# Kernel optimization log

Measured on AMD Instinct MI355X. Metric: run time of the kernel, lower is better.

Reference implementation:

```python
import jax, jax.numpy as jnp
import numpy as np

HID = 128  # args['hidden_size']


def preprocess_adj(A):
    # A: [B, N, N] -> D^{-1/2} (A + I) D^{-1/2}
    N = A.shape[1]
    A_hat = A + jnp.eye(N, dtype=A.dtype)
    d = jnp.sum(A_hat, axis=2)                     # [B, N]
    d_safe = jnp.where(d > 0, d, 1.0)
    d_inv = jnp.where(d > 0, d_safe ** -0.5, 0.0)  # inf -> 0, as in torch code
    return d_inv[:, :, None] * A_hat * d_inv[:, None, :]


def lstm(x, w_ih, w_hh, b_ih, b_hh):
    # x: [B, T, H]; PyTorch gate order i, f, g, o; zero init state
    B = x.shape[0]
    H = w_hh.shape[1]
    def step(carry, xt):
        h, c = carry
        z = xt @ w_ih.T + b_ih + h @ w_hh.T + b_hh
        i, f, g, o = jnp.split(z, 4, axis=-1)
        c = jax.nn.sigmoid(f) * c + jax.nn.sigmoid(i) * jnp.tanh(g)
        h = jax.nn.sigmoid(o) * jnp.tanh(c)
        return (h, c), h
    h0 = jnp.zeros((B, H), x.dtype)
    c0 = jnp.zeros((B, H), x.dtype)
    _, hs = jax.lax.scan(step, (h0, c0), jnp.swapaxes(x, 0, 1))
    return jnp.swapaxes(hs, 0, 1)  # [B, T, H]


def gcn_dynamic_forward(x, A_norm, conv_w, conv_b, w_ih, w_hh, b_ih, b_hh):
    # x: [B, N, HID] with N >= HID: take last HID rows as dynamic-filter input
    df_in = x[:, x.shape[1] - HID:, :]              # [B, HID, HID]
    dyn = jax.lax.conv_general_dilated(
        df_in, conv_w, window_strides=(1,), padding=[(1, 1)],
        dimension_numbers=('NCH', 'OIH', 'NCH')) + conv_b[None, :, None]
    lw = lstm(dyn, w_ih, w_hh, b_ih, b_hh)          # [B, HID, HID]
    agg = jnp.matmul(A_norm, x)                     # [B, N, HID]
    out = jax.nn.sigmoid(jnp.matmul(agg, lw))       # output activation (1-layer GCN)
    return out                                       # dropout is identity in eval


def setup_inputs() -> dict:
    key = jax.random.key(0)
    ks = jax.random.split(key, 8)
    B, N = 4, 4096
    node_embedding = jax.random.normal(ks[0], (B, N, HID), dtype=jnp.float32)
    # sparse symmetric-ish 0/1 adjacency, avg degree ~ N*0.01
    adjacency_matrix = (jax.random.uniform(ks[1], (B, N, N)) < 0.01).astype(jnp.float32)
    s = 0.05
    conv_w = jax.random.normal(ks[2], (HID, HID, 3), dtype=jnp.float32) * s
    conv_b = jax.random.normal(ks[3], (HID,), dtype=jnp.float32) * s
    w_ih = jax.random.normal(ks[4], (4 * HID, HID), dtype=jnp.float32) * s
    w_hh = jax.random.normal(ks[5], (4 * HID, HID), dtype=jnp.float32) * s
    b_ih = jax.random.normal(ks[6], (4 * HID,), dtype=jnp.float32) * s
    b_hh = jax.random.normal(ks[7], (4 * HID,), dtype=jnp.float32) * s
    return {"node_embedding": node_embedding, "adjacency_matrix": adjacency_matrix,
            "conv_w": conv_w, "conv_b": conv_b,
            "w_ih": w_ih, "w_hh": w_hh, "b_ih": b_ih, "b_hh": b_hh}


def reference(node_embedding, adjacency_matrix, conv_w, conv_b, w_ih, w_hh, b_ih, b_hh):
    A_norm = preprocess_adj(adjacency_matrix)
    return gcn_dynamic_forward(node_embedding, A_norm, conv_w, conv_b, w_ih, w_hh, b_ih, b_hh)
```

## Files before the change

kernel.cpp:

```cpp
#include <hip/hip_runtime.h>
#include <math.h>

#define N_NODES 4096
#define HIDN 128
#define MAXNZ 128

typedef float v4f __attribute__((ext_vector_type(4)));
typedef _Float16 h2 __attribute__((ext_vector_type(2)));
typedef _Float16 h8 __attribute__((ext_vector_type(8)));

__device__ __forceinline__ float fsig(float x) { return 1.0f / (1.0f + __expf(-x)); }
__device__ __forceinline__ float ftanh_(float x) { return 1.0f - 2.0f / (__expf(2.0f * x) + 1.0f); }

__global__ __launch_bounds__(512) void k1_conv_ascan(
        const float* __restrict__ x, const float* __restrict__ conv_w,
        const float* __restrict__ conv_b, const float* __restrict__ w_ih,
        const float* __restrict__ b_ih, const float* __restrict__ b_hh,
        float* __restrict__ z3,
        const float* __restrict__ A, float* __restrict__ d_inv,
        int* __restrict__ cnt, int* __restrict__ idx) {
    __shared__ __align__(16) float dyn_lds[4][HIDN];
    __shared__ int sidx[8][MAXNZ];
    if (blockIdx.x < 128) {
        const int cb = blockIdx.x;
        const int b = cb >> 5;
        const int t0 = (cb & 31) * 4;
        const int tsub = threadIdx.x >> 7;
        const int h = threadIdx.x & 127;
        const int t = t0 + tsub;
        {
            const float* xb = x + ((size_t)b * N_NODES + (N_NODES - HIDN)) * HIDN;
            const float* w = conv_w + (size_t)t * HIDN * 3;
            float a0 = conv_b[t], a1 = 0.0f, a2 = 0.0f, a3 = 0.0f;
            #pragma unroll 4
            for (int i = 0; i < HIDN; i += 4) {
                const float* xr0 = xb + (size_t)i * HIDN;
                #pragma unroll
                for (int s = 0; s < 4; ++s) {
                    const float* xr = xr0 + s * HIDN;
                    float w0 = w[(i + s) * 3 + 0], w1 = w[(i + s) * 3 + 1], w2 = w[(i + s) * 3 + 2];
                    float left  = (h > 0)   ? xr[h - 1] : 0.0f;
                    float mid   = xr[h];
                    float right = (h < 127) ? xr[h + 1] : 0.0f;
                    if (s == 0)      a0 += left * w0 + mid * w1 + right * w2;
                    else if (s == 1) a1 += left * w0 + mid * w1 + right * w2;
                    else if (s == 2) a2 += left * w0 + mid * w1 + right * w2;
                    else             a3 += left * w0 + mid * w1 + right * w2;
                }
            }
            dyn_lds[tsub][h] = (a0 + a1) + (a2 + a3);
        }
        __syncthreads();
        const int u = threadIdx.x;
        const int qg = u >> 7;
        const int m  = u & 127;
        const float4* wr = (const float4*)(w_ih + (size_t)u * HIDN);
        float bias = b_ih[u] + b_hh[u];
        float acc0 = bias, acc1 = bias, acc2 = bias, acc3 = bias;
        #pragma unroll
        for (int half = 0; half < 2; ++half) {
            float4 wv[16];
            #pragma unroll
            for (int j = 0; j < 16; ++j) wv[j] = wr[half * 16 + j];
            const float4* d0 = (const float4*)dyn_lds[0] + half * 16;
            const float4* d1 = (const float4*)dyn_lds[1] + half * 16;
            const float4* d2 = (const float4*)dyn_lds[2] + half * 16;
            const float4* d3 = (const float4*)dyn_lds[3] + half * 16;
            #pragma unroll
            for (int j = 0; j < 16; ++j) {
                float4 wj = wv[j];
                float4 v0 = d0[j], v1 = d1[j], v2 = d2[j], v3 = d3[j];
                acc0 += wj.x * v0.x + wj.y * v0.y + wj.z * v0.z + wj.w * v0.w;
                acc1 += wj.x * v1.x + wj.y * v1.y + wj.z * v1.z + wj.w * v1.w;
                acc2 += wj.x * v2.x + wj.y * v2.y + wj.z * v2.z + wj.w * v2.w;
                acc3 += wj.x * v3.x + wj.y * v3.y + wj.z * v3.z + wj.w * v3.w;
            }
        }
        float* zb = z3 + (size_t)b * HIDN * HIDN * 4;
        zb[((size_t)(t0 + 0) * 128 + m) * 4 + qg] = acc0;
        zb[((size_t)(t0 + 1) * 128 + m) * 4 + qg] = acc1;
        zb[((size_t)(t0 + 2) * 128 + m) * 4 + qg] = acc2;
        zb[((size_t)(t0 + 3) * 128 + m) * 4 + qg] = acc3;
    } else {
        const int wid = threadIdx.x >> 6;
        const int lane = threadIdx.x & 63;
        const int r = (blockIdx.x - 128) * 8 + wid;
        const v4f* row = (const v4f*)(A + (size_t)r * N_NODES);
        const unsigned long long below = (1ull << lane) - 1ull;
        int cbase = 0;
        v4f cur[4], nxt[4];
        #pragma unroll
        for (int j = 0; j < 4; ++j) cur[j] = row[j * 64 + lane];
#define PROC1(c, col)                                                         \
        {                                                                     \
            bool nz = ((c) != 0.0f);                                          \
            unsigned long long mm = __ballot(nz);                             \
            if (mm) {                                                         \
                if (nz) {                                                     \
                    int p_ = cbase + __popcll(mm & below);                    \
                    if (p_ < MAXNZ) sidx[wid][p_] = (col);                    \
                }                                                             \
                cbase += __popcll(mm);                                        \
            }                                                                 \
        }
        #pragma unroll
        for (int g = 0; g < 4; ++g) {
            if (g < 3) {
                #pragma unroll
                for (int j = 0; j < 4; ++j) nxt[j] = row[(g + 1) * 256 + j * 64 + lane];
            }
            #pragma unroll
            for (int j = 0; j < 4; ++j) {
                int col0 = ((g * 4 + j) * 64 + lane) * 4;
                PROC1(cur[j].x, col0 + 0);
                PROC1(cur[j].y, col0 + 1);
                PROC1(cur[j].z, col0 + 2);
                PROC1(cur[j].w, col0 + 3);
            }
            #pragma unroll
            for (int j = 0; j < 4; ++j) cur[j] = nxt[j];
        }
#undef PROC1
        int cnt_r = (cbase < MAXNZ) ? cbase : MAXNZ;
        for (int k = lane; k < cnt_r; k += 64)
            idx[r * MAXNZ + k] = sidx[wid][k];
        if (lane == 0) {
            cnt[r] = cnt_r;
            d_inv[r] = rsqrtf((float)(cbase + 1));
        }
    }
}

__global__ __launch_bounds__(512, 2) void k2_lstm_gather(
        const float* __restrict__ z3, const float* __restrict__ w_hh,
        float* __restrict__ lw,
        const float* __restrict__ x, const float* __restrict__ d_inv,
        const int* __restrict__ cnt, const int* __restrict__ idx,
        float* __restrict__ agg) {
    __shared__ __align__(16) float4 zl[16 * 128];
    __shared__ __align__(16) _Float16 hbuf[2][HIDN];
    if (blockIdx.x < 4) {
        const int b = blockIdx.x;
        const int t = threadIdx.x;
        const int m = t >> 2;
        const int q = t & 3;
        h2 w2[4][16];
        #pragma unroll
        for (int g = 0; g < 4; ++g) {
            const float4* wr = (const float4*)(w_hh + ((size_t)(g * HIDN + m)) * HIDN + q * 32);
            #pragma unroll
            for (int j4 = 0; j4 < 8; ++j4) {
                float4 wv = wr[j4];
                w2[g][2 * j4 + 0] = h2{(_Float16)wv.x, (_Float16)wv.y};
                w2[g][2 * j4 + 1] = h2{(_Float16)wv.z, (_Float16)wv.w};
            }
        }
        float c = 0.0f;
        if (t < 64) ((h2*)hbuf[0])[t] = h2{(_Float16)0.0f, (_Float16)0.0f};
        const float4* zsrc = (const float4*)z3 + (size_t)b * 16384;
        float* lwb = lw + (size_t)b * HIDN * HIDN + m;
        float hist[4];
        for (int ch = 0; ch < 8; ++ch) {
            const float4* src = zsrc + ch * 2048;
            #pragma unroll
            for (int k = 0; k < 4; ++k)
                zl[t + 512 * k] = src[t + 512 * k];
            __syncthreads();
            #pragma unroll
            for (int si = 0; si < 16; ++si) {
                const int s = ch * 16 + si;
                const h8* hp = ((const h8*)hbuf[s & 1]) + q * 4;
                h8 H0 = hp[0], H1 = hp[1], H2 = hp[2], H3 = hp[3];
                h2 hh[16];
                #pragma unroll
                for (int j = 0; j < 4; ++j) {
                    hh[j]      = ((const h2*)&H0)[j];
                    hh[4 + j]  = ((const h2*)&H1)[j];
                    hh[8 + j]  = ((const h2*)&H2)[j];
                    hh[12 + j] = ((const h2*)&H3)[j];
                }
                float4 zv = zl[si * 128 + m];
                float a0 = 0.f, a1 = 0.f, a2 = 0.f, a3 = 0.f;
                #pragma unroll
                for (int j = 0; j < 16; ++j) {
                    a0 = __builtin_amdgcn_fdot2(w2[0][j], hh[j], a0, false);
                    a1 = __builtin_amdgcn_fdot2(w2[1][j], hh[j], a1, false);
                    a2 = __builtin_amdgcn_fdot2(w2[2][j], hh[j], a2, false);
                    a3 = __builtin_amdgcn_fdot2(w2[3][j], hh[j], a3, false);
                }
                a0 += __shfl_xor(a0, 1); a0 += __shfl_xor(a0, 2);
                a1 += __shfl_xor(a1, 1); a1 += __shfl_xor(a1, 2);
                a2 += __shfl_xor(a2, 1); a2 += __shfl_xor(a2, 2);
                a3 += __shfl_xor(a3, 1); a3 += __shfl_xor(a3, 2);
                float zi = a0 + zv.x;
                float zf = a1 + zv.y;
                float zg = a2 + zv.z;
                float zo = a3 + zv.w;
                float ig = fsig(zi);
                float fg = fsig(zf);
                float gg = ftanh_(zg);
                float og = fsig(zo);
                c = fg * c + ig * gg;
                float hn = og * ftanh_(c);
                if (q == (si & 3)) hist[si >> 2] = hn;
                if (q == 0) hbuf[(s + 1) & 1][m] = (_Float16)hn;
                __syncthreads();
            }
            #pragma unroll
            for (int j = 0; j < 4; ++j)
                lwb[(size_t)(ch * 16 + q + 4 * j) * HIDN] = hist[j];
        }
    } else {
        const int gIdx = blockIdx.x - 4;
        const int b = (gIdx & 7) >> 1;
        const int o = ((gIdx >> 3) << 1) | (gIdx & 1);
        const int wid = threadIdx.x >> 6;
        const int lane = threadIdx.x & 63;
        float* dl = (float*)zl;
        {
            const float4* dsrc = (const float4*)(d_inv + (b << 12));
            float4* ddst = (float4*)dl;
            ddst[threadIdx.x] = dsrc[threadIdx.x];
            ddst[threadIdx.x + 512] = dsrc[threadIdx.x + 512];
        }
        __syncthreads();
        const int i = o * 8 + wid;
        const int r = (b << 12) + i;
        const float2* xb = (const float2*)(x + (size_t)b * N_NODES * HIDN);
        const int* irow = idx + r * MAXNZ;
        const int n = cnt[r];
        float ax = 0.0f, ay = 0.0f;
        int k = 0;
        for (; k + 8 <= n; k += 8) {
            int4 j0 = *(const int4*)&irow[k];
            int4 j1 = *(const int4*)&irow[k + 4];
            float2 v0 = xb[(size_t)j0.x * 64 + lane];
            float2 v1 = xb[(size_t)j0.y * 64 + lane];
            float2 v2 = xb[(size_t)j0.z * 64 + lane];
            float2 v3 = xb[(size_t)j0.w * 64 + lane];
            float2 v4 = xb[(size_t)j1.x * 64 + lane];
            float2 v5 = xb[(size_t)j1.y * 64 + lane];
            float2 v6 = xb[(size_t)j1.z * 64 + lane];
            float2 v7 = xb[(size_t)j1.w * 64 + lane];
            float d0 = dl[j0.x], d1 = dl[j0.y], d2 = dl[j0.z], d3 = dl[j0.w];
            float d4 = dl[j1.x], d5 = dl[j1.y], d6 = dl[j1.z], d7 = dl[j1.w];
            ax += d0 * v0.x + d1 * v1.x + d2 * v2.x + d3 * v3.x
                + d4 * v4.x + d5 * v5.x + d6 * v6.x + d7 * v7.x;
            ay += d0 * v0.y + d1 * v1.y + d2 * v2.y + d3 * v3.y
                + d4 * v4.y + d5 * v5.y + d6 * v6.y + d7 * v7.y;
        }
        for (; k < n; ++k) {
            int j = irow[k];
            float dj = dl[j];
            float2 v = xb[(size_t)j * 64 + lane];
            ax += dj * v.x;
            ay += dj * v.y;
        }
        float di = dl[i];
        float2 vi = xb[(size_t)i * 64 + lane];
        float2 o2;
        o2.x = di * (ax + di * vi.x);
        o2.y = di * (ay + di * vi.y);
        ((float2*)(agg + (size_t)r * HIDN))[lane] = o2;
    }
}

__global__ __launch_bounds__(256) void k_outmm(
        const float* __restrict__ agg, const float* __restrict__ lw,
        float* __restrict__ out) {
    __shared__ __align__(16) float lw_lds[HIDN * HIDN];
    const int i0 = blockIdx.x * 64;
    const int b = i0 >> 12;
    const float4* lwg = (const float4*)(lw + (size_t)b * HIDN * HIDN);
    float4* lds4 = (float4*)lw_lds;
    for (int v = threadIdx.x; v < HIDN * HIDN / 4; v += 256) lds4[v] = lwg[v];
    __syncthreads();
    const int r0 = i0 + (threadIdx.x >> 3) * 2;
    const int u0 = (threadIdx.x & 7) * 16;
    const float4* a4 = (const float4*)agg;
    float4 acc[2][4];
    #pragma unroll
    for (int rr = 0; rr < 2; ++rr)
        #pragma unroll
        for (int cc = 0; cc < 4; ++cc) acc[rr][cc] = make_float4(0.f, 0.f, 0.f, 0.f);
    for (int f4 = 0; f4 < 32; ++f4) {
        float4 a0 = a4[(size_t)r0 * 32 + f4];
        float4 a1 = a4[(size_t)(r0 + 1) * 32 + f4];
        #pragma unroll
        for (int ff = 0; ff < 4; ++ff) {
            float af0 = (ff == 0) ? a0.x : (ff == 1) ? a0.y : (ff == 2) ? a0.z : a0.w;
            float af1 = (ff == 0) ? a1.x : (ff == 1) ? a1.y : (ff == 2) ? a1.z : a1.w;
            int f = f4 * 4 + ff;
            const float4* wrow = (const float4*)(lw_lds + f * HIDN + u0);
            #pragma unroll
            for (int cc = 0; cc < 4; ++cc) {
                float4 wv = wrow[cc];
                acc[0][cc].x += af0 * wv.x; acc[0][cc].y += af0 * wv.y;
                acc[0][cc].z += af0 * wv.z; acc[0][cc].w += af0 * wv.w;
                acc[1][cc].x += af1 * wv.x; acc[1][cc].y += af1 * wv.y;
                acc[1][cc].z += af1 * wv.z; acc[1][cc].w += af1 * wv.w;
            }
        }
    }
    #pragma unroll
    for (int rr = 0; rr < 2; ++rr) {
        #pragma unroll
        for (int cc = 0; cc < 4; ++cc) {
            float4 ov;
            ov.x = fsig(acc[rr][cc].x);
            ov.y = fsig(acc[rr][cc].y);
            ov.z = fsig(acc[rr][cc].z);
            ov.w = fsig(acc[rr][cc].w);
            *(float4*)(out + (size_t)(r0 + rr) * HIDN + u0 + cc * 4) = ov;
        }
    }
}

extern "C" void kernel_launch(void* const* d_in, const int* in_sizes, int n_in,
                              void* d_out, int out_size, void* d_ws, size_t ws_size,
                              hipStream_t stream) {
    const float* x      = (const float*)d_in[0];
    const float* A      = (const float*)d_in[1];
    const float* conv_w = (const float*)d_in[2];
    const float* conv_b = (const float*)d_in[3];
    const float* w_ih   = (const float*)d_in[4];
    const float* w_hh   = (const float*)d_in[5];
    const float* b_ih   = (const float*)d_in[6];
    const float* b_hh   = (const float*)d_in[7];
    float* out = (float*)d_out;

    char* ws = (char*)d_ws;
    float* d_inv = (float*)ws;
    int*   cnt   = (int*)(ws + 65536);
    int*   idx   = (int*)(ws + 131072);
    float* z3    = (float*)(ws + 131072 + 8388608);
    float* lw    = (float*)(ws + 131072 + 8388608 + 1048576);
    float* agg   = (float*)(ws + 131072 + 8388608 + 1048576 + 262144);

    hipLaunchKernelGGL(k1_conv_ascan, dim3(2176), dim3(512), 0, stream,
                       x, conv_w, conv_b, w_ih, b_ih, b_hh, z3, A, d_inv, cnt, idx);
    hipLaunchKernelGGL(k2_lstm_gather, dim3(2052), dim3(512), 0, stream,
                       z3, w_hh, lw, x, d_inv, cnt, idx, agg);
    hipLaunchKernelGGL(k_outmm, dim3(256), dim3(256), 0, stream, agg, lw, out);
}
```

Baseline: 500.7 us.

## Fuse three kernels into one cooperative persistent kernel with grid syncs

Replaces the three launches with a single cooperative kernel of 512 blocks that runs conv+input-projection and the adjacency scan, then the LSTM and neighbour gather, then the output matmul, separated by grid-wide syncs. Rows are strided across persistent warps instead of one row per warp per block. The aim is to remove launch gaps and inter-kernel drain. In exchange, the gather now reads d_inv from global memory instead of LDS, the output matmul computes one row per thread instead of two, and the three-kernel path is kept as a fallback. The serial LSTM still limits the middle phase while the other blocks wait at the grid barrier.

Result: slower. 840.0 us (+67.8%).

```diff
diff --git a/kernel.cpp b/kernel.cpp
--- a/kernel.cpp
+++ b/kernel.cpp
@@ -1,9 +1,14 @@
 #include <hip/hip_runtime.h>
+#include <hip/hip_cooperative_groups.h>
 #include <math.h>
+
+namespace cg = cooperative_groups;
 
 #define N_NODES 4096
 #define HIDN 128
 #define MAXNZ 128
+#define CGRID 512
+#define NTHR 512
 
 typedef float v4f __attribute__((ext_vector_type(4)));
 typedef _Float16 h2 __attribute__((ext_vector_type(2)));
@@ -12,308 +17,357 @@
 __device__ __forceinline__ float fsig(float x) { return 1.0f / (1.0f + __expf(-x)); }
 __device__ __forceinline__ float ftanh_(float x) { return 1.0f - 2.0f / (__expf(2.0f * x) + 1.0f); }
 
-__global__ __launch_bounds__(512) void k1_conv_ascan(
+
+__device__ __forceinline__ void convz_body(
+        int cb, int tid, const float* __restrict__ x,
+        const float* __restrict__ conv_w, const float* __restrict__ conv_b,
+        const float* __restrict__ w_ih, const float* __restrict__ b_ih,
+        const float* __restrict__ b_hh, float* __restrict__ z3,
+        float* dl ) {
+    const int b = cb >> 5;
+    const int t0 = (cb & 31) * 4;
+    const int tsub = tid >> 7;
+    const int h = tid & 127;
+    const int t = t0 + tsub;
+    {
+        const float* xb = x + ((size_t)b * N_NODES + (N_NODES - HIDN)) * HIDN;
+        const float* w = conv_w + (size_t)t * HIDN * 3;
+        float a0 = conv_b[t], a1 = 0.0f, a2 = 0.0f, a3 = 0.0f;
+        #pragma unroll 4
+        for (int i = 0; i < HIDN; i += 4) {
+            const float* xr0 = xb + (size_t)i * HIDN;
+            #pragma unroll
+            for (int s = 0; s < 4; ++s) {
+                const float* xr = xr0 + s * HIDN;
+                float w0 = w[(i + s) * 3 + 0], w1 = w[(i + s) * 3 + 1], w2 = w[(i + s) * 3 + 2];
+                float left  = (h > 0)   ? xr[h - 1] : 0.0f;
+                float mid   = xr[h];
+                float right = (h < 127) ? xr[h + 1] : 0.0f;
+                if (s == 0)      a0 += left * w0 + mid * w1 + right * w2;
+                else if (s == 1) a1 += left * w0 + mid * w1 + right * w2;
+                else if (s == 2) a2 += left * w0 + mid * w1 + right * w2;
+                else             a3 += left * w0 + mid * w1 + right * w2;
+            }
+        }
+        dl[tsub * HIDN + h] = (a0 + a1) + (a2 + a3);
+    }
+    __syncthreads();
+    const int u = tid;
+    const int qg = u >> 7;
+    const int m  = u & 127;
+    const float4* wr = (const float4*)(w_ih + (size_t)u * HIDN);
+    float bias = b_ih[u] + b_hh[u];
+    float acc0 = bias, acc1 = bias, acc2 = bias, acc3 = bias;
+    #pragma unroll
+    for (int half = 0; half < 2; ++half) {
+        float4 wv[16];
+        #pragma unroll
+        for (int j = 0; j < 16; ++j) wv[j] = wr[half * 16 + j];
+        const float4* d0 = (const float4*)(dl + 0 * HIDN) + half * 16;
+        const float4* d1 = (const float4*)(dl + 1 * HIDN) + half * 16;
+        const float4* d2 = (const float4*)(dl + 2 * HIDN) + half * 16;
+        const float4* d3 = (const float4*)(dl + 3 * HIDN) + half * 16;
+        #pragma unroll
+        for (int j = 0; j < 16; ++j) {
+            float4 wj = wv[j];
+            float4 v0 = d0[j], v1 = d1[j], v2 = d2[j], v3 = d3[j];
+            acc0 += wj.x * v0.x + wj.y * v0.y + wj.z * v0.z + wj.w * v0.w;
+            acc1 += wj.x * v1.x + wj.y * v1.y + wj.z * v1.z + wj.w * v1.w;
+            acc2 += wj.x * v2.x + wj.y * v2.y + wj.z * v2.z + wj.w * v2.w;
+            acc3 += wj.x * v3.x + wj.y * v3.y + wj.z * v3.z + wj.w * v3.w;
+        }
+    }
+    float* zb = z3 + (size_t)b * HIDN * HIDN * 4;
+    zb[((size_t)(t0 + 0) * 128 + m) * 4 + qg] = acc0;
+    zb[((size_t)(t0 + 1) * 128 + m) * 4 + qg] = acc1;
+    zb[((size_t)(t0 + 2) * 128 + m) * 4 + qg] = acc2;
+    zb[((size_t)(t0 + 3) * 128 + m) * 4 + qg] = acc3;
+}
+
+__device__ __forceinline__ void ascan_row(
+        int r, int lane, const float* __restrict__ A, float* __restrict__ d_inv,
+        int* __restrict__ cnt, int* __restrict__ idx, int* sidx_w) {
+    const v4f* row = (const v4f*)(A + (size_t)r * N_NODES);
+    const unsigned long long below = (1ull << lane) - 1ull;
+    int cbase = 0;
+    v4f cur[4], nxt[4];
+    #pragma unroll
+    for (int j = 0; j < 4; ++j) cur[j] = row[j * 64 + lane];
+#define PROC1(c, col)                                                         \
+    {                                                                         \
+        bool nz = ((c) != 0.0f);                                              \
+        unsigned long long mm = __ballot(nz);                                 \
+        if (mm) {                                                             \
+            if (nz) {                                                         \
+                int p_ = cbase + __popcll(mm & below);                        \
+                if (p_ < MAXNZ) sidx_w[p_] = (col);                           \
+            }                                                                 \
+            cbase += __popcll(mm);                                            \
+        }                                                                     \
+    }
+    #pragma unroll
+    for (int g = 0; g < 4; ++g) {
+        if (g < 3) {
+            #pragma unroll
+            for (int j = 0; j < 4; ++j) nxt[j] = row[(g + 1) * 256 + j * 64 + lane];
+        }
+        #pragma unroll
+        for (int j = 0; j < 4; ++j) {
+            int col0 = ((g * 4 + j) * 64 + lane) * 4;
+            PROC1(cur[j].x, col0 + 0);
+            PROC1(cur[j].y, col0 + 1);
+            PROC1(cur[j].z, col0 + 2);
+            PROC1(cur[j].w, col0 + 3);
+        }
+        #pragma unroll
+        for (int j = 0; j < 4; ++j) cur[j] = nxt[j];
+    }
+#undef PROC1
+    int cnt_r = (cbase < MAXNZ) ? cbase : MAXNZ;
+    for (int k = lane; k < cnt_r; k += 64)
+        idx[r * MAXNZ + k] = sidx_w[k];
+    if (lane == 0) {
+        cnt[r] = cnt_r;
+        d_inv[r] = rsqrtf((float)(cbase + 1));
+    }
+}
+
+__device__ __forceinline__ void lstm_body(
+        int b, int t, const float* __restrict__ z3, const float* __restrict__ w_hh,
+        float* __restrict__ lw, float4* zl, _Float16* hb) {
+    const int m = t >> 2;
+    const int q = t & 3;
+    h2 w2[4][16];
+    #pragma unroll
+    for (int g = 0; g < 4; ++g) {
+        const float4* wr = (const float4*)(w_hh + ((size_t)(g * HIDN + m)) * HIDN + q * 32);
+        #pragma unroll
+        for (int j4 = 0; j4 < 8; ++j4) {
+            float4 wv = wr[j4];
+            w2[g][2 * j4 + 0] = h2{(_Float16)wv.x, (_Float16)wv.y};
+            w2[g][2 * j4 + 1] = h2{(_Float16)wv.z, (_Float16)wv.w};
+        }
+    }
+    float c = 0.0f;
+    if (t < 64) ((h2*)hb)[t] = h2{(_Float16)0.0f, (_Float16)0.0f};
+    const float4* zsrc = (const float4*)z3 + (size_t)b * 16384;
+    float* lwb = lw + (size_t)b * HIDN * HIDN + m;
+    float hist[4];
+    for (int ch = 0; ch < 8; ++ch) {
+        const float4* src = zsrc + ch * 2048;
+        #pragma unroll
+        for (int k = 0; k < 4; ++k)
+            zl[t + 512 * k] = src[t + 512 * k];
+        __syncthreads();
+        #pragma unroll
+        for (int si = 0; si < 16; ++si) {
+            const int s = ch * 16 + si;
+            const h8* hp = ((const h8*)(hb + (size_t)(s & 1) * HIDN)) + q * 4;
+            h8 H0 = hp[0], H1 = hp[1], H2 = hp[2], H3 = hp[3];
+            float4 zv = zl[si * 128 + m];
+            float a0 = 0.f, a1 = 0.f, a2 = 0.f, a3 = 0.f;
+            #pragma unroll
+            for (int j = 0; j < 16; ++j) {
+                h2 hj = (j < 4)  ? ((const h2*)&H0)[j]
+                      : (j < 8)  ? ((const h2*)&H1)[j - 4]
+                      : (j < 12) ? ((const h2*)&H2)[j - 8]
+                                 : ((const h2*)&H3)[j - 12];
+                a0 = __builtin_amdgcn_fdot2(w2[0][j], hj, a0, false);
+                a1 = __builtin_amdgcn_fdot2(w2[1][j], hj, a1, false);
+                a2 = __builtin_amdgcn_fdot2(w2[2][j], hj, a2, false);
+                a3 = __builtin_amdgcn_fdot2(w2[3][j], hj, a3, false);
+            }
+            a0 += __shfl_xor(a0, 1); a0 += __shfl_xor(a0, 2);
+            a1 += __shfl_xor(a1, 1); a1 += __shfl_xor(a1, 2);
+            a2 += __shfl_xor(a2, 1); a2 += __shfl_xor(a2, 2);
+            a3 += __shfl_xor(a3, 1); a3 += __shfl_xor(a3, 2);
+            float zi = a0 + zv.x;
+            float zf = a1 + zv.y;
+            float zg = a2 + zv.z;
+            float zo = a3 + zv.w;
+            float ig = fsig(zi);
+            float fg = fsig(zf);
+            float gg = ftanh_(zg);
+            float og = fsig(zo);
+            c = fg * c + ig * gg;
+            float hn = og * ftanh_(c);
+            if (q == (si & 3)) hist[si >> 2] = hn;
+            if (q == 0) hb[(size_t)((s + 1) & 1) * HIDN + m] = (_Float16)hn;
+            __syncthreads();
+        }
+        #pragma unroll
+        for (int j = 0; j < 4; ++j)
+            lwb[(size_t)(ch * 16 + q + 4 * j) * HIDN] = hist[j];
+    }
+}
+
+__device__ __forceinline__ void gather_row(
+        int r, int lane, const float* __restrict__ x,
+        const float* __restrict__ d_inv, const int* __restrict__ cnt,
+        const int* __restrict__ idx, float* __restrict__ agg) {
+    const int b = r >> 12;
+    const int i = r & 4095;
+    const float* dv = d_inv + (b << 12);
+    const float2* xb = (const float2*)(x + (size_t)b * N_NODES * HIDN);
+    const int* irow = idx + r * MAXNZ;
+    const int n = cnt[r];
+    float ax = 0.0f, ay = 0.0f;
+    int k = 0;
+    for (; k + 8 <= n; k += 8) {
+        int4 j0 = *(const int4*)&irow[k];
+        int4 j1 = *(const int4*)&irow[k + 4];
+        float2 v0 = xb[(size_t)j0.x * 64 + lane];
+        float2 v1 = xb[(size_t)j0.y * 64 + lane];
+        float2 v2 = xb[(size_t)j0.z * 64 + lane];
+        float2 v3 = xb[(size_t)j0.w * 64 + lane];
+        float2 v4 = xb[(size_t)j1.x * 64 + lane];
+        float2 v5 = xb[(size_t)j1.y * 64 + lane];
+        float2 v6 = xb[(size_t)j1.z * 64 + lane];
+        float2 v7 = xb[(size_t)j1.w * 64 + lane];
+        float d0 = dv[j0.x], d1 = dv[j0.y], d2 = dv[j0.z], d3 = dv[j0.w];
+        float d4 = dv[j1.x], d5 = dv[j1.y], d6 = dv[j1.z], d7 = dv[j1.w];
+        ax += d0 * v0.x + d1 * v1.x + d2 * v2.x + d3 * v3.x
+            + d4 * v4.x + d5 * v5.x + d6 * v6.x + d7 * v7.x;
+        ay += d0 * v0.y + d1 * v1.y + d2 * v2.y + d3 * v3.y
+            + d4 * v4.y + d5 * v5.y + d6 * v6.y + d7 * v7.y;
+    }
+    for (; k < n; ++k) {
+        int j = irow[k];
+        float dj = dv[j];
+        float2 v = xb[(size_t)j * 64 + lane];
+        ax += dj * v.x;
+        ay += dj * v.y;
+    }
+    float di = dv[i];
+    float2 vi = xb[(size_t)i * 64 + lane];
+    float2 o2;
+    o2.x = di * (ax + di * vi.x);
+    o2.y = di * (ay + di * vi.y);
+    ((float2*)(agg + (size_t)r * HIDN))[lane] = o2;
+}
+
+__device__ __forceinline__ void outmm_body(
+        int bb, int tid, const float* __restrict__ agg,
+        const float* __restrict__ lw, float* __restrict__ out, float* lw_lds) {
+    const int i0 = bb * 64;
+    const int b = i0 >> 12;
+    const float4* lwg = (const float4*)(lw + (size_t)b * HIDN * HIDN);
+    float4* lds4 = (float4*)lw_lds;
+    for (int v = tid; v < HIDN * HIDN / 4; v += NTHR) lds4[v] = lwg[v];
+    __syncthreads();
+    const int r0 = i0 + (tid >> 3);
+    const int u0 = (tid & 7) * 16;
+    const float4* a4 = (const float4*)agg;
+    float4 acc[4];
+    #pragma unroll
+    for (int cc = 0; cc < 4; ++cc) acc[cc] = make_float4(0.f, 0.f, 0.f, 0.f);
+    for (int f4 = 0; f4 < 32; ++f4) {
+        float4 a0 = a4[(size_t)r0 * 32 + f4];
+        #pragma unroll
+        for (int ff = 0; ff < 4; ++ff) {
+            float af0 = (ff == 0) ? a0.x : (ff == 1) ? a0.y : (ff == 2) ? a0.z : a0.w;
+            const float4* wrow = (const float4*)(lw_lds + (f4 * 4 + ff) * HIDN + u0);
+            #pragma unroll
+            for (int cc = 0; cc < 4; ++cc) {
+                float4 wv = wrow[cc];
+                acc[cc].x += af0 * wv.x; acc[cc].y += af0 * wv.y;
+                acc[cc].z += af0 * wv.z; acc[cc].w += af0 * wv.w;
+            }
+        }
+    }
+    #pragma unroll
+    for (int cc = 0; cc < 4; ++cc) {
+        float4 ov;
+        ov.x = fsig(acc[cc].x);
+        ov.y = fsig(acc[cc].y);
+        ov.z = fsig(acc[cc].z);
+        ov.w = fsig(acc[cc].w);
+        *(float4*)(out + (size_t)r0 * HIDN + u0 + cc * 4) = ov;
+    }
+}
+
+__global__ __launch_bounds__(NTHR, 4) void k_fused(
+        const float* __restrict__ x, const float* __restrict__ A,
+        const float* __restrict__ conv_w, const float* __restrict__ conv_b,
+        const float* __restrict__ w_ih, const float* __restrict__ w_hh,
+        const float* __restrict__ b_ih, const float* __restrict__ b_hh,
+        float* __restrict__ z3, float* __restrict__ d_inv,
+        int* __restrict__ cnt, int* __restrict__ idx,
+        float* __restrict__ lw, float* __restrict__ agg,
+        float* __restrict__ out) {
+    __shared__ __align__(16) char arena[65536];
+    cg::grid_group grid = cg::this_grid();
+    const int tid = threadIdx.x;
+    const int bid = blockIdx.x;
+    const int wid = tid >> 6;
+    const int lane = tid & 63;
+
+    if (bid < 128) {
+        convz_body(bid, tid, x, conv_w, conv_b, w_ih, b_ih, b_hh, z3, (float*)arena);
+    } else {
+        int* sidx_w = (int*)arena + wid * MAXNZ;
+        const int gw = (bid - 128) * 8 + wid;
+        for (int r = gw; r < 16384; r += 3072)
+            ascan_row(r, lane, A, d_inv, cnt, idx, sidx_w);
+    }
+    __threadfence();
+    grid.sync();
+
+    if (bid < 4) {
+        lstm_body(bid, tid, z3, w_hh, lw, (float4*)arena, (_Float16*)(arena + 32768));
+    } else {
+        const int gw = (bid - 4) * 8 + wid;
+        for (int r = gw; r < 16384; r += 4064)
+            gather_row(r, lane, x, d_inv, cnt, idx, agg);
+    }
+    __threadfence();
+    grid.sync();
+
+    if (bid < 256)
+        outmm_body(bid, tid, agg, lw, out, (float*)arena);
+}
+
+__global__ __launch_bounds__(512) void k1_fb(
         const float* __restrict__ x, const float* __restrict__ conv_w,
         const float* __restrict__ conv_b, const float* __restrict__ w_ih,
         const float* __restrict__ b_ih, const float* __restrict__ b_hh,
         float* __restrict__ z3,
         const float* __restrict__ A, float* __restrict__ d_inv,
         int* __restrict__ cnt, int* __restrict__ idx) {
-    __shared__ __align__(16) float dyn_lds[4][HIDN];
-    __shared__ int sidx[8][MAXNZ];
+    __shared__ __align__(16) char arena[4096];
     if (blockIdx.x < 128) {
-        const int cb = blockIdx.x;
-        const int b = cb >> 5;
-        const int t0 = (cb & 31) * 4;
-        const int tsub = threadIdx.x >> 7;
-        const int h = threadIdx.x & 127;
-        const int t = t0 + tsub;
-        {
-            const float* xb = x + ((size_t)b * N_NODES + (N_NODES - HIDN)) * HIDN;
-            const float* w = conv_w + (size_t)t * HIDN * 3;
-            float a0 = conv_b[t], a1 = 0.0f, a2 = 0.0f, a3 = 0.0f;
-            #pragma unroll 4
-            for (int i = 0; i < HIDN; i += 4) {
-                const float* xr0 = xb + (size_t)i * HIDN;
-                #pragma unroll
-                for (int s = 0; s < 4; ++s) {
-                    const float* xr = xr0 + s * HIDN;
-                    float w0 = w[(i + s) * 3 + 0], w1 = w[(i + s) * 3 + 1], w2 = w[(i + s) * 3 + 2];
-                    float left  = (h > 0)   ? xr[h - 1] : 0.0f;
-                    float mid   = xr[h];
-                    float right = (h < 127) ? xr[h + 1] : 0.0f;
-                    if (s == 0)      a0 += left * w0 + mid * w1 + right * w2;
-                    else if (s == 1) a1 += left * w0 + mid * w1 + right * w2;
-                    else if (s == 2) a2 += left * w0 + mid * w1 + right * w2;
-                    else             a3 += left * w0 + mid * w1 + right * w2;
-                }
-            }
-            dyn_lds[tsub][h] = (a0 + a1) + (a2 + a3);
-        }
-        __syncthreads();
-        const int u = threadIdx.x;
-        const int qg = u >> 7;
-        const int m  = u & 127;
-        const float4* wr = (const float4*)(w_ih + (size_t)u * HIDN);
-        float bias = b_ih[u] + b_hh[u];
-        float acc0 = bias, acc1 = bias, acc2 = bias, acc3 = bias;
-        #pragma unroll
-        for (int half = 0; half < 2; ++half) {
-            float4 wv[16];
-            #pragma unroll
-            for (int j = 0; j < 16; ++j) wv[j] = wr[half * 16 + j];
-            const float4* d0 = (const float4*)dyn_lds[0] + half * 16;
-            const float4* d1 = (const float4*)dyn_lds[1] + half * 16;
-            const float4* d2 = (const float4*)dyn_lds[2] + half * 16;
-            const float4* d3 = (const float4*)dyn_lds[3] + half * 16;
-            #pragma unroll
-            for (int j = 0; j < 16; ++j) {
-                float4 wj = wv[j];
-                float4 v0 = d0[j], v1 = d1[j], v2 = d2[j], v3 = d3[j];
-                acc0 += wj.x * v0.x + wj.y * v0.y + wj.z * v0.z + wj.w * v0.w;
-                acc1 += wj.x * v1.x + wj.y * v1.y + wj.z * v1.z + wj.w * v1.w;
-                acc2 += wj.x * v2.x + wj.y * v2.y + wj.z * v2.z + wj.w * v2.w;
-                acc3 += wj.x * v3.x + wj.y * v3.y + wj.z * v3.z + wj.w * v3.w;
-            }
-        }
-        float* zb = z3 + (size_t)b * HIDN * HIDN * 4;
-        zb[((size_t)(t0 + 0) * 128 + m) * 4 + qg] = acc0;
-        zb[((size_t)(t0 + 1) * 128 + m) * 4 + qg] = acc1;
-        zb[((size_t)(t0 + 2) * 128 + m) * 4 + qg] = acc2;
-        zb[((size_t)(t0 + 3) * 128 + m) * 4 + qg] = acc3;
+        convz_body(blockIdx.x, threadIdx.x, x, conv_w, conv_b, w_ih, b_ih, b_hh,
+                   z3, (float*)arena);
     } else {
         const int wid = threadIdx.x >> 6;
         const int lane = threadIdx.x & 63;
-        const int r = (blockIdx.x - 128) * 8 + wid;
-        const v4f* row = (const v4f*)(A + (size_t)r * N_NODES);
-        const unsigned long long below = (1ull << lane) - 1ull;
-        int cbase = 0;
-        v4f cur[4], nxt[4];
-        #pragma unroll
-        for (int j = 0; j < 4; ++j) cur[j] = row[j * 64 + lane];
-#define PROC1(c, col)                                                         \
-        {                                                                     \
-            bool nz = ((c) != 0.0f);                                          \
-            unsigned long long mm = __ballot(nz);                             \
-            if (mm) {                                                         \
-                if (nz) {                                                     \
-                    int p_ = cbase + __popcll(mm & below);                    \
-                    if (p_ < MAXNZ) sidx[wid][p_] = (col);                    \
-                }                                                             \
-                cbase += __popcll(mm);                                        \
-            }                                                                 \
-        }
-        #pragma unroll
-        for (int g = 0; g < 4; ++g) {
-            if (g < 3) {
-                #pragma unroll
-                for (int j = 0; j < 4; ++j) nxt[j] = row[(g + 1) * 256 + j * 64 + lane];
-            }
-            #pragma unroll
-            for (int j = 0; j < 4; ++j) {
-                int col0 = ((g * 4 + j) * 64 + lane) * 4;
-                PROC1(cur[j].x, col0 + 0);
-                PROC1(cur[j].y, col0 + 1);
-                PROC1(cur[j].z, col0 + 2);
-                PROC1(cur[j].w, col0 + 3);
-            }
-            #pragma unroll
-            for (int j = 0; j < 4; ++j) cur[j] = nxt[j];
-        }
-#undef PROC1
-        int cnt_r = (cbase < MAXNZ) ? cbase : MAXNZ;
-        for (int k = lane; k < cnt_r; k += 64)
-            idx[r * MAXNZ + k] = sidx[wid][k];
-        if (lane == 0) {
-            cnt[r] = cnt_r;
-            d_inv[r] = rsqrtf((float)(cbase + 1));
-        }
-    }
-}
-
-__global__ __launch_bounds__(512, 2) void k2_lstm_gather(
+        int* sidx_w = (int*)arena + wid * MAXNZ;
+        ascan_row((blockIdx.x - 128) * 8 + wid, lane, A, d_inv, cnt, idx, sidx_w);
+    }
+}
+
+__global__ __launch_bounds__(512) void k2_fb(
         const float* __restrict__ z3, const float* __restrict__ w_hh,
         float* __restrict__ lw,
         const float* __restrict__ x, const float* __restrict__ d_inv,
         const int* __restrict__ cnt, const int* __restrict__ idx,
         float* __restrict__ agg) {
-    __shared__ __align__(16) float4 zl[16 * 128];
-    __shared__ __align__(16) _Float16 hbuf[2][HIDN];
+    __shared__ __align__(16) char arena[33280];
     if (blockIdx.x < 4) {
-        const int b = blockIdx.x;
-        const int t = threadIdx.x;
-        const int m = t >> 2;
-        const int q = t & 3;
-        h2 w2[4][16];
-        #pragma unroll
-        for (int g = 0; g < 4; ++g) {
-            const float4* wr = (const float4*)(w_hh + ((size_t)(g * HIDN + m)) * HIDN + q * 32);
-            #pragma unroll
-            for (int j4 = 0; j4 < 8; ++j4) {
-                float4 wv = wr[j4];
-                w2[g][2 * j4 + 0] = h2{(_Float16)wv.x, (_Float16)wv.y};
-                w2[g][2 * j4 + 1] = h2{(_Float16)wv.z, (_Float16)wv.w};
-            }
-        }
-        float c = 0.0f;
-        if (t < 64) ((h2*)hbuf[0])[t] = h2{(_Float16)0.0f, (_Float16)0.0f};
-        const float4* zsrc = (const float4*)z3 + (size_t)b * 16384;
-        float* lwb = lw + (size_t)b * HIDN * HIDN + m;
-        float hist[4];
-        for (int ch = 0; ch < 8; ++ch) {
-            const float4* src = zsrc + ch * 2048;
-            #pragma unroll
-            for (int k = 0; k < 4; ++k)
-                zl[t + 512 * k] = src[t + 512 * k];
-            __syncthreads();
-            #pragma unroll
-            for (int si = 0; si < 16; ++si) {
-                const int s = ch * 16 + si;
-                const h8* hp = ((const h8*)hbuf[s & 1]) + q * 4;
-                h8 H0 = hp[0], H1 = hp[1], H2 = hp[2], H3 = hp[3];
-                h2 hh[16];
-                #pragma unroll
-                for (int j = 0; j < 4; ++j) {
-                    hh[j]      = ((const h2*)&H0)[j];
-                    hh[4 + j]  = ((const h2*)&H1)[j];
-                    hh[8 + j]  = ((const h2*)&H2)[j];
-                    hh[12 + j] = ((const h2*)&H3)[j];
-                }
-                float4 zv = zl[si * 128 + m];
-                float a0 = 0.f, a1 = 0.f, a2 = 0.f, a3 = 0.f;
-                #pragma unroll
-                for (int j = 0; j < 16; ++j) {
-                    a0 = __builtin_amdgcn_fdot2(w2[0][j], hh[j], a0, false);
-                    a1 = __builtin_amdgcn_fdot2(w2[1][j], hh[j], a1, false);
-                    a2 = __builtin_amdgcn_fdot2(w2[2][j], hh[j], a2, false);
-                    a3 = __builtin_amdgcn_fdot2(w2[3][j], hh[j], a3, false);
-                }
-                a0 += __shfl_xor(a0, 1); a0 += __shfl_xor(a0, 2);
-                a1 += __shfl_xor(a1, 1); a1 += __shfl_xor(a1, 2);
-                a2 += __shfl_xor(a2, 1); a2 += __shfl_xor(a2, 2);
-                a3 += __shfl_xor(a3, 1); a3 += __shfl_xor(a3, 2);
-                float zi = a0 + zv.x;
-                float zf = a1 + zv.y;
-                float zg = a2 + zv.z;
-                float zo = a3 + zv.w;
-                float ig = fsig(zi);
-                float fg = fsig(zf);
-                float gg = ftanh_(zg);
-                float og = fsig(zo);
-                c = fg * c + ig * gg;
-                float hn = og * ftanh_(c);
-                if (q == (si & 3)) hist[si >> 2] = hn;
-                if (q == 0) hbuf[(s + 1) & 1][m] = (_Float16)hn;
-                __syncthreads();
-            }
-            #pragma unroll
-            for (int j = 0; j < 4; ++j)
-                lwb[(size_t)(ch * 16 + q + 4 * j) * HIDN] = hist[j];
-        }
+        lstm_body(blockIdx.x, threadIdx.x, z3, w_hh, lw,
+                  (float4*)arena, (_Float16*)(arena + 32768));
     } else {
-        const int gIdx = blockIdx.x - 4;
-        const int b = (gIdx & 7) >> 1;
-        const int o = ((gIdx >> 3) << 1) | (gIdx & 1);
         const int wid = threadIdx.x >> 6;
         const int lane = threadIdx.x & 63;
-        float* dl = (float*)zl;
-        {
-            const float4* dsrc = (const float4*)(d_inv + (b << 12));
-            float4* ddst = (float4*)dl;
-            ddst[threadIdx.x] = dsrc[threadIdx.x];
-            ddst[threadIdx.x + 512] = dsrc[threadIdx.x + 512];
-        }
-        __syncthreads();
-        const int i = o * 8 + wid;
-        const int r = (b << 12) + i;
-        const float2* xb = (const float2*)(x + (size_t)b * N_NODES * HIDN);
-        const int* irow = idx + r * MAXNZ;
-        const int n = cnt[r];
-        float ax = 0.0f, ay = 0.0f;
-        int k = 0;
-        for (; k + 8 <= n; k += 8) {
-            int4 j0 = *(const int4*)&irow[k];
-            int4 j1 = *(const int4*)&irow[k + 4];
-            float2 v0 = xb[(size_t)j0.x * 64 + lane];
-            float2 v1 = xb[(size_t)j0.y * 64 + lane];
-            float2 v2 = xb[(size_t)j0.z * 64 + lane];
-            float2 v3 = xb[(size_t)j0.w * 64 + lane];
-            float2 v4 = xb[(size_t)j1.x * 64 + lane];
-            float2 v5 = xb[(size_t)j1.y * 64 + lane];
-            float2 v6 = xb[(size_t)j1.z * 64 + lane];
-            float2 v7 = xb[(size_t)j1.w * 64 + lane];
-            float d0 = dl[j0.x], d1 = dl[j0.y], d2 = dl[j0.z], d3 = dl[j0.w];
-            float d4 = dl[j1.x], d5 = dl[j1.y], d6 = dl[j1.z], d7 = dl[j1.w];
-            ax += d0 * v0.x + d1 * v1.x + d2 * v2.x + d3 * v3.x
-                + d4 * v4.x + d5 * v5.x + d6 * v6.x + d7 * v7.x;
-            ay += d0 * v0.y + d1 * v1.y + d2 * v2.y + d3 * v3.y
-                + d4 * v4.y + d5 * v5.y + d6 * v6.y + d7 * v7.y;
-        }
-        for (; k < n; ++k) {
-            int j = irow[k];
-            float dj = dl[j];
-            float2 v = xb[(size_t)j * 64 + lane];
-            ax += dj * v.x;
-            ay += dj * v.y;
-        }
-        float di = dl[i];
-        float2 vi = xb[(size_t)i * 64 + lane];
-        float2 o2;
-        o2.x = di * (ax + di * vi.x);
-        o2.y = di * (ay + di * vi.y);
-        ((float2*)(agg + (size_t)r * HIDN))[lane] = o2;
-    }
-}
-
-__global__ __launch_bounds__(256) void k_outmm(
+        gather_row((blockIdx.x - 4) * 8 + wid, lane, x, d_inv, cnt, idx, agg);
+    }
+}
+
+__global__ __launch_bounds__(512) void k3_fb(
         const float* __restrict__ agg, const float* __restrict__ lw,
         float* __restrict__ out) {
-    __shared__ __align__(16) float lw_lds[HIDN * HIDN];
-    const int i0 = blockIdx.x * 64;
-    const int b = i0 >> 12;
-    const float4* lwg = (const float4*)(lw + (size_t)b * HIDN * HIDN);
-    float4* lds4 = (float4*)lw_lds;
-    for (int v = threadIdx.x; v < HIDN * HIDN / 4; v += 256) lds4[v] = lwg[v];
-    __syncthreads();
-    const int r0 = i0 + (threadIdx.x >> 3) * 2;
-    const int u0 = (threadIdx.x & 7) * 16;
-    const float4* a4 = (const float4*)agg;
-    float4 acc[2][4];
-    #pragma unroll
-    for (int rr = 0; rr < 2; ++rr)
-        #pragma unroll
-        for (int cc = 0; cc < 4; ++cc) acc[rr][cc] = make_float4(0.f, 0.f, 0.f, 0.f);
-    for (int f4 = 0; f4 < 32; ++f4) {
-        float4 a0 = a4[(size_t)r0 * 32 + f4];
-        float4 a1 = a4[(size_t)(r0 + 1) * 32 + f4];
-        #pragma unroll
-        for (int ff = 0; ff < 4; ++ff) {
-            float af0 = (ff == 0) ? a0.x : (ff == 1) ? a0.y : (ff == 2) ? a0.z : a0.w;
-            float af1 = (ff == 0) ? a1.x : (ff == 1) ? a1.y : (ff == 2) ? a1.z : a1.w;
-            int f = f4 * 4 + ff;
-            const float4* wrow = (const float4*)(lw_lds + f * HIDN + u0);
-            #pragma unroll
-            for (int cc = 0; cc < 4; ++cc) {
-                float4 wv = wrow[cc];
-                acc[0][cc].x += af0 * wv.x; acc[0][cc].y += af0 * wv.y;
-                acc[0][cc].z += af0 * wv.z; acc[0][cc].w += af0 * wv.w;
-                acc[1][cc].x += af1 * wv.x; acc[1][cc].y += af1 * wv.y;
-                acc[1][cc].z += af1 * wv.z; acc[1][cc].w += af1 * wv.w;
-            }
-        }
-    }
-    #pragma unroll
-    for (int rr = 0; rr < 2; ++rr) {
-        #pragma unroll
-        for (int cc = 0; cc < 4; ++cc) {
-            float4 ov;
-            ov.x = fsig(acc[rr][cc].x);
-            ov.y = fsig(acc[rr][cc].y);
-            ov.z = fsig(acc[rr][cc].z);
-            ov.w = fsig(acc[rr][cc].w);
-            *(float4*)(out + (size_t)(r0 + rr) * HIDN + u0 + cc * 4) = ov;
-        }
-    }
+    __shared__ __align__(16) char arena[65536];
+    outmm_body(blockIdx.x, threadIdx.x, agg, lw, out, (float*)arena);
 }
 
 extern "C" void kernel_launch(void* const* d_in, const int* in_sizes, int n_in,
@@ -337,9 +391,19 @@
     float* lw    = (float*)(ws + 131072 + 8388608 + 1048576);
     float* agg   = (float*)(ws + 131072 + 8388608 + 1048576 + 262144);
 
-    hipLaunchKernelGGL(k1_conv_ascan, dim3(2176), dim3(512), 0, stream,
-                       x, conv_w, conv_b, w_ih, b_ih, b_hh, z3, A, d_inv, cnt, idx);
-    hipLaunchKernelGGL(k2_lstm_gather, dim3(2052), dim3(512), 0, stream,
-                       z3, w_hh, lw, x, d_inv, cnt, idx, agg);
-    hipLaunchKernelGGL(k_outmm, dim3(256), dim3(256), 0, stream, agg, lw, out);
-}
+    void* args[] = {
+        (void*)&x, (void*)&A, (void*)&conv_w, (void*)&conv_b,
+        (void*)&w_ih, (void*)&w_hh, (void*)&b_ih, (void*)&b_hh,
+        (void*)&z3, (void*)&d_inv, (void*)&cnt, (void*)&idx,
+        (void*)&lw, (void*)&agg, (void*)&out,
+    };
+    hipError_t err = hipLaunchCooperativeKernel(
+        (const void*)k_fused, dim3(CGRID), dim3(NTHR), (void**)args, 0, stream);
+    if (err != hipSuccess) {
+        hipLaunchKernelGGL(k1_fb, dim3(2176), dim3(512), 0, stream,
+                           x, conv_w, conv_b, w_ih, b_ih, b_hh, z3, A, d_inv, cnt, idx);
+        hipLaunchKernelGGL(k2_fb, dim3(2052), dim3(512), 0, stream,
+                           z3, w_hh, lw, x, d_inv, cnt, idx, agg);
+        hipLaunchKernelGGL(k3_fb, dim3(256), dim3(512), 0, stream, agg, lw, out);
+    }
+}
```
